# Kernel optimization log

Hardware: AMD Instinct MI355X
Metric: run time of the kernel (lower is better)

## Reference

```python
import jax, jax.numpy as jnp
import numpy as np


def setup_inputs() -> dict:
    key = jax.random.key(0)
    ks = jax.random.split(key, 5)
    B, S, H, F, E = 2, 2048, 768, 1536, 8
    scale_h = 1.0 / np.sqrt(H)
    scale_f = 1.0 / np.sqrt(F)
    return {
        "hidden_states": jax.random.normal(ks[0], (B, S, H), dtype=jnp.float32),
        "gate_w": jax.random.normal(ks[1], (E, H), dtype=jnp.float32) * scale_h,
        "w1": jax.random.normal(ks[2], (E, F, H), dtype=jnp.float32) * scale_h,
        "w3": jax.random.normal(ks[3], (E, F, H), dtype=jnp.float32) * scale_h,
        "w2": jax.random.normal(ks[4], (E, H, F), dtype=jnp.float32) * scale_f,
        "k": 2,
    }


def reference(hidden_states, gate_w, w1, w3, w2, k):
    B, S, H = hidden_states.shape
    E = gate_w.shape[0]
    x = hidden_states.reshape(-1, H)                     # [T, H]
    T = x.shape[0]

    # Router: softmax in fp32, top-k, renormalize among selected experts.
    router_logits = x @ gate_w.T                         # [T, E]
    probs = jax.nn.softmax(router_logits.astype(jnp.float32), axis=-1)
    top_w, top_i = jax.lax.top_k(probs, k)               # [T, k]
    top_w = top_w / jnp.sum(top_w, axis=-1, keepdims=True)
    top_w = top_w.astype(x.dtype)

    # Scatter top-k weights into dense [T, E] combine weights (0 for unselected).
    combine = jnp.zeros((T, E), dtype=x.dtype)
    combine = combine.at[jnp.arange(T)[:, None], top_i].set(top_w)

    # SwiGLU experts (zero-weight experts contribute exactly 0 to the sum).
    g = jnp.einsum("th,efh->tef", x, w1)                 # [T, E, F]
    u = jnp.einsum("th,efh->tef", x, w3)                 # [T, E, F]
    act = jax.nn.silu(g) * u                             # [T, E, F]
    expert_out = jnp.einsum("tef,ehf->teh", act, w2)     # [T, E, H]
    y = jnp.einsum("te,teh->th", combine, expert_out)    # [T, H]

    return y.reshape(B, S, H), router_logits
```

## Files before the change

### kernel.cpp

```cpp
#include <hip/hip_runtime.h>
#include <hip/hip_bf16.h>

#define T_TOK 4096
#define H_DIM 768
#define E_NUM 8
#define F_DIM 1536
#define WELEM (E_NUM * F_DIM * H_DIM)

typedef __bf16 bf16x8 __attribute__((ext_vector_type(8)));
typedef float f32x4 __attribute__((ext_vector_type(4)));
typedef unsigned int u32;

#define VMCNT(n) asm volatile("s_waitcnt vmcnt(" #n ")" ::: "memory")
#define CFENCE() asm volatile("" ::: "memory")

__device__ __forceinline__ unsigned short f2bf(float f) {
    unsigned int u = __float_as_uint(f);
    u += 0x7FFF + ((u >> 16) & 1);
    return (unsigned short)(u >> 16);
}

__device__ __forceinline__ void gload16(const unsigned short* g, unsigned short* l) {
    __builtin_amdgcn_global_load_lds(
        (const __attribute__((address_space(1))) u32*)(g),
        (__attribute__((address_space(3))) u32*)(l),
        16, 0, 0);
}

__global__ void convert3_kernel(const float* __restrict__ s0,
                                const float* __restrict__ s1,
                                const float* __restrict__ s2,
                                unsigned short* __restrict__ d0,
                                unsigned short* __restrict__ d1,
                                unsigned short* __restrict__ d2) {
    int i = (blockIdx.x * blockDim.x + threadIdx.x) * 4;
    int stride = gridDim.x * blockDim.x * 4;
    for (; i < 3 * WELEM; i += stride) {
        int r = i / WELEM;
        int j = i - r * WELEM;
        const float* s = (r == 0) ? s0 : (r == 1) ? s1 : s2;
        unsigned short* d = (r == 0) ? d0 : (r == 1) ? d1 : d2;
        float4 v = *reinterpret_cast<const float4*>(s + j);
        ushort4 o;
        o.x = f2bf(v.x); o.y = f2bf(v.y); o.z = f2bf(v.z); o.w = f2bf(v.w);
        *reinterpret_cast<ushort4*>(d + j) = o;
    }
}

__global__ __launch_bounds__(256) void router_kernel(
    const float* __restrict__ x,
    const float* __restrict__ gw,
    float* __restrict__ logits_out,
    float* __restrict__ weight,
    int* __restrict__ eidx,
    unsigned short* __restrict__ xb) {
    int t = blockIdx.x * 4 + (threadIdx.x >> 6);
    int lane = threadIdx.x & 63;

    const float4* xr = reinterpret_cast<const float4*>(x + (size_t)t * H_DIM);
    float4 xv[3];
#pragma unroll
    for (int i = 0; i < 3; ++i) xv[i] = xr[i * 64 + lane];

    unsigned short* xbr = xb + (size_t)t * H_DIM;
#pragma unroll
    for (int i = 0; i < 3; ++i) {
        ushort4 o;
        o.x = f2bf(xv[i].x); o.y = f2bf(xv[i].y);
        o.z = f2bf(xv[i].z); o.w = f2bf(xv[i].w);
        *reinterpret_cast<ushort4*>(xbr + (i * 64 + lane) * 4) = o;
    }

    float v[E_NUM];
#pragma unroll
    for (int e = 0; e < E_NUM; ++e) {
        const float4* g = reinterpret_cast<const float4*>(gw + e * H_DIM);
        float p = 0.f;
#pragma unroll
        for (int i = 0; i < 3; ++i) {
            float4 gv = g[i * 64 + lane];
            p += xv[i].x * gv.x + xv[i].y * gv.y + xv[i].z * gv.z + xv[i].w * gv.w;
        }
        v[e] = p;
    }
#pragma unroll
    for (int d = 1; d < 8; d <<= 1)
#pragma unroll
        for (int e = 0; e < E_NUM; ++e) v[e] += __shfl_xor(v[e], d);
    int me = lane & 7;
    float le = v[0];
#pragma unroll
    for (int e = 1; e < E_NUM; ++e) le = (me == e) ? v[e] : le;
#pragma unroll
    for (int d = 8; d < 64; d <<= 1) le += __shfl_xor(le, d);

    if (lane < 8) logits_out[t * E_NUM + lane] = le;

    float m0 = le;
#pragma unroll
    for (int d = 1; d < 8; d <<= 1) m0 = fmaxf(m0, __shfl_xor(m0, d));
    unsigned long long b0 = __ballot(le == m0);
    int e0 = (__ffsll((long long)b0) - 1) & 7;
    float le1 = (me == e0) ? -3.4e38f : le;
    float m1 = le1;
#pragma unroll
    for (int d = 1; d < 8; d <<= 1) m1 = fmaxf(m1, __shfl_xor(m1, d));
    unsigned long long b1 = __ballot(le1 == m1);
    int e1 = (__ffsll((long long)b1) - 1) & 7;

    if (lane == 0) {
        float w0 = 1.f / (1.f + __expf(m1 - m0));
        weight[t * 2 + 0] = w0;
        weight[t * 2 + 1] = 1.f - w0;
        eidx[t] = e0 | (e1 << 8);
    }
}

__global__ __launch_bounds__(256) void build_lists_kernel(
    const int* __restrict__ eidx,
    int* __restrict__ list,
    int* __restrict__ counts) {
    int e = blockIdx.x;
    int tid = threadIdx.x;
    int lane = tid & 63;
    int wv = tid >> 6;
    __shared__ int wsum[4];
    __shared__ int wbase[4];
    __shared__ int sbase;
    if (tid == 0) sbase = 0;
    __syncthreads();
    for (int c = 0; c < T_TOK; c += 256) {
        int tok = c + tid;
        int pk = eidx[tok];
        int slot = -1;
        if ((pk & 255) == e) slot = tok * 2;
        else if ((pk >> 8) == e) slot = tok * 2 + 1;
        unsigned long long m = __ballot(slot >= 0);
        int prefix = __popcll(m & ((1ull << lane) - 1ull));
        if (lane == 0) wsum[wv] = __popcll(m);
        __syncthreads();
        if (tid == 0) {
            int s = sbase;
#pragma unroll
            for (int i = 0; i < 4; ++i) { wbase[i] = s; s += wsum[i]; }
            sbase = s;
        }
        __syncthreads();
        if (slot >= 0) list[e * T_TOK + wbase[wv] + prefix] = slot;
        __syncthreads();
    }
    if (tid == 0) counts[e] = sbase;
}

__global__ __launch_bounds__(256, 3) void gemm13_kernel(
    const unsigned short* __restrict__ xb,
    const unsigned short* __restrict__ w1b,
    const unsigned short* __restrict__ w3b,
    const int* __restrict__ list,
    const int* __restrict__ counts,
    unsigned short* __restrict__ act) {
    int orig = blockIdx.x;
    int wg = (orig & 7) * 768 + (orig >> 3);
    int tm = wg & 31;
    int tn = (wg >> 5) % 24;
    int e = wg / (32 * 24);

    int cnt = counts[e];
    if (tm * 128 >= cnt) return;
    const int* lst = list + e * T_TOK + tm * 128;
    int mrem = cnt - tm * 128;

    __shared__ unsigned short sA[3][128 * 32];
    __shared__ unsigned short sB1[3][64 * 32];
    __shared__ unsigned short sB3[3][64 * 32];

    int tid = threadIdx.x;
    int lane = tid & 63;
    int wid = tid >> 6;

    int r0 = tid >> 2;
    int r1 = r0 + 64;
    int c8 = ((tid & 3) ^ ((r0 >> 1) & 3)) * 8;
    int tok0 = lst[(r0 < mrem) ? r0 : 0] >> 1;
    int tok1 = lst[(r1 < mrem) ? r1 : 0] >> 1;
    const unsigned short* gA0 = xb + (size_t)tok0 * H_DIM + c8;
    const unsigned short* gA1 = xb + (size_t)tok1 * H_DIM + c8;
    const unsigned short* gB1 = w1b + ((size_t)e * F_DIM + tn * 64 + r0) * H_DIM + c8;
    const unsigned short* gB3 = w3b + ((size_t)e * F_DIM + tn * 64 + r0) * H_DIM + c8;

    auto stage = [&](int b, int kt) {
        gload16(gA0 + kt, &sA[b][wid * 512]);
        gload16(gA1 + kt, &sA[b][2048 + wid * 512]);
        gload16(gB1 + kt, &sB1[b][wid * 512]);
        gload16(gB3 + kt, &sB3[b][wid * 512]);
    };

    int wr = (wid >> 1) * 64;
    int wc = (wid & 1) * 32;
    int fr = lane & 15;
    int kb = ((lane >> 4) ^ ((lane >> 1) & 3)) * 8;

    f32x4 accG[4][2] = {};
    f32x4 accU[4][2] = {};

    const int NT = H_DIM / 32;
    stage(0, 0);
    stage(1, 32);
    VMCNT(4);
    __builtin_amdgcn_s_barrier();
    CFENCE();
    int cur = 0;
    for (int t = 0; t < NT; ++t) {
        if (t + 2 < NT) {
            int nb = cur + 2; if (nb >= 3) nb -= 3;
            stage(nb, (t + 2) * 32);
        }
        CFENCE();

        bf16x8 a[4], b1[2], b3[2];
#pragma unroll
        for (int mi = 0; mi < 4; ++mi)
            a[mi] = *reinterpret_cast<const bf16x8*>(&sA[cur][(wr + mi * 16 + fr) * 32 + kb]);
#pragma unroll
        for (int ni = 0; ni < 2; ++ni) {
            b1[ni] = *reinterpret_cast<const bf16x8*>(&sB1[cur][(wc + ni * 16 + fr) * 32 + kb]);
            b3[ni] = *reinterpret_cast<const bf16x8*>(&sB3[cur][(wc + ni * 16 + fr) * 32 + kb]);
        }
#pragma unroll
        for (int mi = 0; mi < 4; ++mi)
#pragma unroll
            for (int ni = 0; ni < 2; ++ni) {
                accG[mi][ni] = __builtin_amdgcn_mfma_f32_16x16x32_bf16(a[mi], b1[ni], accG[mi][ni], 0, 0, 0);
                accU[mi][ni] = __builtin_amdgcn_mfma_f32_16x16x32_bf16(a[mi], b3[ni], accU[mi][ni], 0, 0, 0);
            }
        CFENCE();
        if (t + 2 < NT) { VMCNT(4); } else { VMCNT(0); }
        __builtin_amdgcn_s_barrier();
        CFENCE();
        cur = (cur + 1 < 3) ? cur + 1 : 0;
    }

    int rg = (lane >> 4) * 4;
    int ci = lane & 15;
#pragma unroll
    for (int mi = 0; mi < 4; ++mi) {
#pragma unroll
        for (int r = 0; r < 4; ++r) {
            int m = wr + mi * 16 + rg + r;
            if (m >= mrem) continue;
            int entry = lst[m];
            size_t rowOff = (size_t)entry * F_DIM + tn * 64;
#pragma unroll
            for (int ni = 0; ni < 2; ++ni) {
                float g = accG[mi][ni][r];
                float u = accU[mi][ni][r];
                float s = g / (1.f + __expf(-g));
                act[rowOff + wc + ni * 16 + ci] = f2bf(s * u);
            }
        }
    }
}

__global__ __launch_bounds__(256, 3) void gemm2_kernel(
    const unsigned short* __restrict__ act,
    const unsigned short* __restrict__ w2b,
    const int* __restrict__ list,
    const int* __restrict__ counts,
    const float* __restrict__ weight,
    float* __restrict__ ybuf) {
    int orig = blockIdx.x;
    int wg = (orig & 7) * 192 + (orig >> 3);
    int tm = wg & 31;
    int tn = (wg >> 5) % 6;
    int e = wg / (32 * 6);

    int cnt = counts[e];
    if (tm * 128 >= cnt) return;
    const int* lst = list + e * T_TOK + tm * 128;
    int mrem = cnt - tm * 128;

    __shared__ unsigned short sA[3][128 * 32];
    __shared__ unsigned short sB[3][128 * 32];

    int tid = threadIdx.x;
    int lane = tid & 63;
    int wid = tid >> 6;

    int r0 = tid >> 2;
    int r1 = r0 + 64;
    int c8 = ((tid & 3) ^ ((r0 >> 1) & 3)) * 8;
    int row0 = lst[(r0 < mrem) ? r0 : 0];
    int row1 = lst[(r1 < mrem) ? r1 : 0];
    const unsigned short* gA0 = act + (size_t)row0 * F_DIM + c8;
    const unsigned short* gA1 = act + (size_t)row1 * F_DIM + c8;
    const unsigned short* gB0 = w2b + ((size_t)e * H_DIM + tn * 128 + r0) * F_DIM + c8;
    const unsigned short* gB1 = gB0 + (size_t)64 * F_DIM;

    auto stage = [&](int b, int kt) {
        gload16(gA0 + kt, &sA[b][wid * 512]);
        gload16(gA1 + kt, &sA[b][2048 + wid * 512]);
        gload16(gB0 + kt, &sB[b][wid * 512]);
        gload16(gB1 + kt, &sB[b][2048 + wid * 512]);
    };

    int wr = (wid >> 1) * 64;
    int wc = (wid & 1) * 64;
    int fr = lane & 15;
    int kb = ((lane >> 4) ^ ((lane >> 1) & 3)) * 8;

    f32x4 acc[4][4] = {};

    const int NT = F_DIM / 32;
    stage(0, 0);
    stage(1, 32);
    VMCNT(4);
    __builtin_amdgcn_s_barrier();
    CFENCE();
    int cur = 0;
    for (int t = 0; t < NT; ++t) {
        if (t + 2 < NT) {
            int nb = cur + 2; if (nb >= 3) nb -= 3;
            stage(nb, (t + 2) * 32);
        }
        CFENCE();

        bf16x8 a[4], b[4];
#pragma unroll
        for (int mi = 0; mi < 4; ++mi)
            a[mi] = *reinterpret_cast<const bf16x8*>(&sA[cur][(wr + mi * 16 + fr) * 32 + kb]);
#pragma unroll
        for (int ni = 0; ni < 4; ++ni)
            b[ni] = *reinterpret_cast<const bf16x8*>(&sB[cur][(wc + ni * 16 + fr) * 32 + kb]);
#pragma unroll
        for (int mi = 0; mi < 4; ++mi)
#pragma unroll
            for (int ni = 0; ni < 4; ++ni)
                acc[mi][ni] = __builtin_amdgcn_mfma_f32_16x16x32_bf16(a[mi], b[ni], acc[mi][ni], 0, 0, 0);
        CFENCE();
        if (t + 2 < NT) { VMCNT(4); } else { VMCNT(0); }
        __builtin_amdgcn_s_barrier();
        CFENCE();
        cur = (cur + 1 < 3) ? cur + 1 : 0;
    }

    int rg = (lane >> 4) * 4;
    int ci = lane & 15;
#pragma unroll
    for (int mi = 0; mi < 4; ++mi) {
#pragma unroll
        for (int r = 0; r < 4; ++r) {
            int m = wr + mi * 16 + rg + r;
            if (m >= mrem) continue;
            int entry = lst[m];
            float wv = weight[entry];
            size_t rowOff = (size_t)entry * H_DIM + tn * 128;
#pragma unroll
            for (int ni = 0; ni < 4; ++ni)
                ybuf[rowOff + wc + ni * 16 + ci] = acc[mi][ni][r] * wv;
        }
    }
}

__global__ void combine_kernel(const float* __restrict__ ybuf, float* __restrict__ y) {
    int v = blockIdx.x * blockDim.x + threadIdx.x;
    if (v >= T_TOK * H_DIM / 4) return;
    int t = v / (H_DIM / 4);
    int hv = v % (H_DIM / 4);
    float4 a = reinterpret_cast<const float4*>(ybuf + (size_t)(2 * t) * H_DIM)[hv];
    float4 b = reinterpret_cast<const float4*>(ybuf + (size_t)(2 * t + 1) * H_DIM)[hv];
    float4 r;
    r.x = a.x + b.x; r.y = a.y + b.y; r.z = a.z + b.z; r.w = a.w + b.w;
    reinterpret_cast<float4*>(y)[v] = r;
}

extern "C" void kernel_launch(void* const* d_in, const int* in_sizes, int n_in,
                              void* d_out, int out_size, void* d_ws, size_t ws_size,
                              hipStream_t stream) {
    const float* x  = (const float*)d_in[0];
    const float* gw = (const float*)d_in[1];
    const float* w1 = (const float*)d_in[2];
    const float* w3 = (const float*)d_in[3];
    const float* w2 = (const float*)d_in[4];

    float* y = (float*)d_out;
    float* logits_out = y + (size_t)T_TOK * H_DIM;

    char* ws = (char*)d_ws;
    size_t off = 0;
    auto alloc = [&](size_t bytes) -> char* {
        char* p = ws + off;
        off += (bytes + 255) & ~(size_t)255;
        return p;
    };
    unsigned short* xb  = (unsigned short*)alloc((size_t)T_TOK * H_DIM * 2);
    unsigned short* w1b = (unsigned short*)alloc((size_t)WELEM * 2);
    unsigned short* w3b = (unsigned short*)alloc((size_t)WELEM * 2);
    unsigned short* w2b = (unsigned short*)alloc((size_t)WELEM * 2);
    unsigned short* act = (unsigned short*)alloc((size_t)T_TOK * 2 * F_DIM * 2);
    float* ybuf   = (float*)alloc((size_t)T_TOK * 2 * H_DIM * 4);
    float* weight = (float*)alloc((size_t)T_TOK * 2 * 4);
    int* list     = (int*)alloc((size_t)E_NUM * T_TOK * 4);
    int* counts   = (int*)alloc((size_t)E_NUM * 4);
    int* eidx     = (int*)alloc((size_t)T_TOK * 4);

    convert3_kernel<<<4096, 256, 0, stream>>>(w1, w3, w2, w1b, w3b, w2b);

    router_kernel<<<T_TOK / 4, 256, 0, stream>>>(x, gw, logits_out, weight, eidx, xb);

    build_lists_kernel<<<E_NUM, 256, 0, stream>>>(eidx, list, counts);

    gemm13_kernel<<<6144, 256, 0, stream>>>(xb, w1b, w3b, list, counts, act);

    gemm2_kernel<<<1536, 256, 0, stream>>>(act, w2b, list, counts, weight, ybuf);

    combine_kernel<<<(T_TOK * H_DIM / 4 + 255) / 256, 256, 0, stream>>>(ybuf, y);
}
```

Measured before the change: 159.6 us.

## Switch GEMM pipelines to BK=64 double buffering with 8-chunk XOR swizzle

Both expert GEMM kernels move from a three-stage, K=32 LDS pipeline to a two-stage, K=64 double buffer. The LDS layout now uses a 64-wide row with an 8-way XOR swizzle, and each tile runs two MFMA sub-steps. MFMA sections are wrapped in s_setprio raises, and occupancy hints drop from 3 to 2 blocks per CU. This halves the number of barriers and loop iterations per K. In exchange, only one tile is prefetched ahead, so latency is hidden less, and occupancy is lower because more LDS is used.

```diff
diff --git a/kernel.cpp b/kernel.cpp
--- a/kernel.cpp
+++ b/kernel.cpp
@@ -152,7 +152,7 @@
     if (tid == 0) counts[e] = sbase;
 }
 
-__global__ __launch_bounds__(256, 3) void gemm13_kernel(
+__global__ __launch_bounds__(256, 2) void gemm13_kernel(
     const unsigned short* __restrict__ xb,
     const unsigned short* __restrict__ w1b,
     const unsigned short* __restrict__ w3b,
@@ -170,74 +170,90 @@
     const int* lst = list + e * T_TOK + tm * 128;
     int mrem = cnt - tm * 128;
 
-    __shared__ unsigned short sA[3][128 * 32];
-    __shared__ unsigned short sB1[3][64 * 32];
-    __shared__ unsigned short sB3[3][64 * 32];
+    __shared__ unsigned short sA[2][128 * 64];
+    __shared__ unsigned short sB1[2][64 * 64];
+    __shared__ unsigned short sB3[2][64 * 64];
 
     int tid = threadIdx.x;
     int lane = tid & 63;
     int wid = tid >> 6;
 
-    int r0 = tid >> 2;
-    int r1 = r0 + 64;
-    int c8 = ((tid & 3) ^ ((r0 >> 1) & 3)) * 8;
-    int tok0 = lst[(r0 < mrem) ? r0 : 0] >> 1;
-    int tok1 = lst[(r1 < mrem) ? r1 : 0] >> 1;
-    const unsigned short* gA0 = xb + (size_t)tok0 * H_DIM + c8;
-    const unsigned short* gA1 = xb + (size_t)tok1 * H_DIM + c8;
-    const unsigned short* gB1 = w1b + ((size_t)e * F_DIM + tn * 64 + r0) * H_DIM + c8;
-    const unsigned short* gB3 = w3b + ((size_t)e * F_DIM + tn * 64 + r0) * H_DIM + c8;
+    int rs = tid >> 3;
+    int cs = tid & 7;
+    int ra0 = rs, ra1 = rs + 32, ra2 = rs + 64, ra3 = rs + 96;
+    int tokA0 = lst[(ra0 < mrem) ? ra0 : 0] >> 1;
+    int tokA1 = lst[(ra1 < mrem) ? ra1 : 0] >> 1;
+    int tokA2 = lst[(ra2 < mrem) ? ra2 : 0] >> 1;
+    int tokA3 = lst[(ra3 < mrem) ? ra3 : 0] >> 1;
+    const unsigned short* gA0 = xb + (size_t)tokA0 * H_DIM + ((cs ^ (ra0 & 7)) << 3);
+    const unsigned short* gA1 = xb + (size_t)tokA1 * H_DIM + ((cs ^ (ra1 & 7)) << 3);
+    const unsigned short* gA2 = xb + (size_t)tokA2 * H_DIM + ((cs ^ (ra2 & 7)) << 3);
+    const unsigned short* gA3 = xb + (size_t)tokA3 * H_DIM + ((cs ^ (ra3 & 7)) << 3);
+    const unsigned short* gB1a = w1b + ((size_t)e * F_DIM + tn * 64 + ra0) * H_DIM + ((cs ^ (ra0 & 7)) << 3);
+    const unsigned short* gB1b = w1b + ((size_t)e * F_DIM + tn * 64 + ra1) * H_DIM + ((cs ^ (ra1 & 7)) << 3);
+    const unsigned short* gB3a = w3b + ((size_t)e * F_DIM + tn * 64 + ra0) * H_DIM + ((cs ^ (ra0 & 7)) << 3);
+    const unsigned short* gB3b = w3b + ((size_t)e * F_DIM + tn * 64 + ra1) * H_DIM + ((cs ^ (ra1 & 7)) << 3);
 
     auto stage = [&](int b, int kt) {
-        gload16(gA0 + kt, &sA[b][wid * 512]);
-        gload16(gA1 + kt, &sA[b][2048 + wid * 512]);
-        gload16(gB1 + kt, &sB1[b][wid * 512]);
-        gload16(gB3 + kt, &sB3[b][wid * 512]);
+        gload16(gA0 + kt, &sA[b][0 * 2048 + wid * 512]);
+        gload16(gA1 + kt, &sA[b][1 * 2048 + wid * 512]);
+        gload16(gA2 + kt, &sA[b][2 * 2048 + wid * 512]);
+        gload16(gA3 + kt, &sA[b][3 * 2048 + wid * 512]);
+        gload16(gB1a + kt, &sB1[b][0 * 2048 + wid * 512]);
+        gload16(gB1b + kt, &sB1[b][1 * 2048 + wid * 512]);
+        gload16(gB3a + kt, &sB3[b][0 * 2048 + wid * 512]);
+        gload16(gB3b + kt, &sB3[b][1 * 2048 + wid * 512]);
     };
 
     int wr = (wid >> 1) * 64;
     int wc = (wid & 1) * 32;
     int fr = lane & 15;
-    int kb = ((lane >> 4) ^ ((lane >> 1) & 3)) * 8;
+    int f7 = fr & 7;
+    int kq = lane >> 4;
 
     f32x4 accG[4][2] = {};
     f32x4 accU[4][2] = {};
 
-    const int NT = H_DIM / 32;
+    const int NT = H_DIM / 64;
     stage(0, 0);
-    stage(1, 32);
-    VMCNT(4);
+    VMCNT(0);
     __builtin_amdgcn_s_barrier();
     CFENCE();
     int cur = 0;
     for (int t = 0; t < NT; ++t) {
-        if (t + 2 < NT) {
-            int nb = cur + 2; if (nb >= 3) nb -= 3;
-            stage(nb, (t + 2) * 32);
-        }
+        if (t + 1 < NT) stage(cur ^ 1, (t + 1) * 64);
         CFENCE();
 
-        bf16x8 a[4], b1[2], b3[2];
-#pragma unroll
-        for (int mi = 0; mi < 4; ++mi)
-            a[mi] = *reinterpret_cast<const bf16x8*>(&sA[cur][(wr + mi * 16 + fr) * 32 + kb]);
-#pragma unroll
-        for (int ni = 0; ni < 2; ++ni) {
-            b1[ni] = *reinterpret_cast<const bf16x8*>(&sB1[cur][(wc + ni * 16 + fr) * 32 + kb]);
-            b3[ni] = *reinterpret_cast<const bf16x8*>(&sB3[cur][(wc + ni * 16 + fr) * 32 + kb]);
-        }
-#pragma unroll
-        for (int mi = 0; mi < 4; ++mi)
+#pragma unroll
+        for (int kh = 0; kh < 2; ++kh) {
+            int cA = kh * 4 + kq;
+            int koff = ((cA ^ f7) << 3);
+            bf16x8 a[4], b1[2], b3[2];
+#pragma unroll
+            for (int mi = 0; mi < 4; ++mi)
+                a[mi] = *reinterpret_cast<const bf16x8*>(&sA[cur][(wr + mi * 16 + fr) * 64 + koff]);
 #pragma unroll
             for (int ni = 0; ni < 2; ++ni) {
-                accG[mi][ni] = __builtin_amdgcn_mfma_f32_16x16x32_bf16(a[mi], b1[ni], accG[mi][ni], 0, 0, 0);
-                accU[mi][ni] = __builtin_amdgcn_mfma_f32_16x16x32_bf16(a[mi], b3[ni], accU[mi][ni], 0, 0, 0);
+                b1[ni] = *reinterpret_cast<const bf16x8*>(&sB1[cur][(wc + ni * 16 + fr) * 64 + koff]);
+                b3[ni] = *reinterpret_cast<const bf16x8*>(&sB3[cur][(wc + ni * 16 + fr) * 64 + koff]);
             }
+            __builtin_amdgcn_s_setprio(1);
+#pragma unroll
+            for (int mi = 0; mi < 4; ++mi)
+#pragma unroll
+                for (int ni = 0; ni < 2; ++ni) {
+                    accG[mi][ni] = __builtin_amdgcn_mfma_f32_16x16x32_bf16(a[mi], b1[ni], accG[mi][ni], 0, 0, 0);
+                    accU[mi][ni] = __builtin_amdgcn_mfma_f32_16x16x32_bf16(a[mi], b3[ni], accU[mi][ni], 0, 0, 0);
+                }
+            __builtin_amdgcn_s_setprio(0);
+        }
         CFENCE();
-        if (t + 2 < NT) { VMCNT(4); } else { VMCNT(0); }
-        __builtin_amdgcn_s_barrier();
-        CFENCE();
-        cur = (cur + 1 < 3) ? cur + 1 : 0;
+        if (t + 1 < NT) {
+            VMCNT(0);
+            __builtin_amdgcn_s_barrier();
+            CFENCE();
+        }
+        cur ^= 1;
     }
 
     int rg = (lane >> 4) * 4;
@@ -261,7 +277,7 @@
     }
 }
 
-__global__ __launch_bounds__(256, 3) void gemm2_kernel(
+__global__ __launch_bounds__(256, 2) void gemm2_kernel(
     const unsigned short* __restrict__ act,
     const unsigned short* __restrict__ w2b,
     const int* __restrict__ list,
@@ -279,68 +295,84 @@
     const int* lst = list + e * T_TOK + tm * 128;
     int mrem = cnt - tm * 128;
 
-    __shared__ unsigned short sA[3][128 * 32];
-    __shared__ unsigned short sB[3][128 * 32];
+    __shared__ unsigned short sA[2][128 * 64];
+    __shared__ unsigned short sB[2][128 * 64];
 
     int tid = threadIdx.x;
     int lane = tid & 63;
     int wid = tid >> 6;
 
-    int r0 = tid >> 2;
-    int r1 = r0 + 64;
-    int c8 = ((tid & 3) ^ ((r0 >> 1) & 3)) * 8;
-    int row0 = lst[(r0 < mrem) ? r0 : 0];
-    int row1 = lst[(r1 < mrem) ? r1 : 0];
-    const unsigned short* gA0 = act + (size_t)row0 * F_DIM + c8;
-    const unsigned short* gA1 = act + (size_t)row1 * F_DIM + c8;
-    const unsigned short* gB0 = w2b + ((size_t)e * H_DIM + tn * 128 + r0) * F_DIM + c8;
-    const unsigned short* gB1 = gB0 + (size_t)64 * F_DIM;
+    int rs = tid >> 3;
+    int cs = tid & 7;
+    int ra0 = rs, ra1 = rs + 32, ra2 = rs + 64, ra3 = rs + 96;
+    int rowA0 = lst[(ra0 < mrem) ? ra0 : 0];
+    int rowA1 = lst[(ra1 < mrem) ? ra1 : 0];
+    int rowA2 = lst[(ra2 < mrem) ? ra2 : 0];
+    int rowA3 = lst[(ra3 < mrem) ? ra3 : 0];
+    const unsigned short* gA0 = act + (size_t)rowA0 * F_DIM + ((cs ^ (ra0 & 7)) << 3);
+    const unsigned short* gA1 = act + (size_t)rowA1 * F_DIM + ((cs ^ (ra1 & 7)) << 3);
+    const unsigned short* gA2 = act + (size_t)rowA2 * F_DIM + ((cs ^ (ra2 & 7)) << 3);
+    const unsigned short* gA3 = act + (size_t)rowA3 * F_DIM + ((cs ^ (ra3 & 7)) << 3);
+    const unsigned short* gB0 = w2b + ((size_t)e * H_DIM + tn * 128 + ra0) * F_DIM + ((cs ^ (ra0 & 7)) << 3);
+    const unsigned short* gB1 = w2b + ((size_t)e * H_DIM + tn * 128 + ra1) * F_DIM + ((cs ^ (ra1 & 7)) << 3);
+    const unsigned short* gB2 = w2b + ((size_t)e * H_DIM + tn * 128 + ra2) * F_DIM + ((cs ^ (ra2 & 7)) << 3);
+    const unsigned short* gB3 = w2b + ((size_t)e * H_DIM + tn * 128 + ra3) * F_DIM + ((cs ^ (ra3 & 7)) << 3);
 
     auto stage = [&](int b, int kt) {
-        gload16(gA0 + kt, &sA[b][wid * 512]);
-        gload16(gA1 + kt, &sA[b][2048 + wid * 512]);
-        gload16(gB0 + kt, &sB[b][wid * 512]);
-        gload16(gB1 + kt, &sB[b][2048 + wid * 512]);
+        gload16(gA0 + kt, &sA[b][0 * 2048 + wid * 512]);
+        gload16(gA1 + kt, &sA[b][1 * 2048 + wid * 512]);
+        gload16(gA2 + kt, &sA[b][2 * 2048 + wid * 512]);
+        gload16(gA3 + kt, &sA[b][3 * 2048 + wid * 512]);
+        gload16(gB0 + kt, &sB[b][0 * 2048 + wid * 512]);
+        gload16(gB1 + kt, &sB[b][1 * 2048 + wid * 512]);
+        gload16(gB2 + kt, &sB[b][2 * 2048 + wid * 512]);
+        gload16(gB3 + kt, &sB[b][3 * 2048 + wid * 512]);
     };
 
     int wr = (wid >> 1) * 64;
     int wc = (wid & 1) * 64;
     int fr = lane & 15;
-    int kb = ((lane >> 4) ^ ((lane >> 1) & 3)) * 8;
+    int f7 = fr & 7;
+    int kq = lane >> 4;
 
     f32x4 acc[4][4] = {};
 
-    const int NT = F_DIM / 32;
+    const int NT = F_DIM / 64;
     stage(0, 0);
-    stage(1, 32);
-    VMCNT(4);
+    VMCNT(0);
     __builtin_amdgcn_s_barrier();
     CFENCE();
     int cur = 0;
     for (int t = 0; t < NT; ++t) {
-        if (t + 2 < NT) {
-            int nb = cur + 2; if (nb >= 3) nb -= 3;
-            stage(nb, (t + 2) * 32);
-        }
+        if (t + 1 < NT) stage(cur ^ 1, (t + 1) * 64);
         CFENCE();
 
-        bf16x8 a[4], b[4];
-#pragma unroll
-        for (int mi = 0; mi < 4; ++mi)
-            a[mi] = *reinterpret_cast<const bf16x8*>(&sA[cur][(wr + mi * 16 + fr) * 32 + kb]);
-#pragma unroll
-        for (int ni = 0; ni < 4; ++ni)
-            b[ni] = *reinterpret_cast<const bf16x8*>(&sB[cur][(wc + ni * 16 + fr) * 32 + kb]);
-#pragma unroll
-        for (int mi = 0; mi < 4; ++mi)
+#pragma unroll
+        for (int kh = 0; kh < 2; ++kh) {
+            int cA = kh * 4 + kq;
+            int koff = ((cA ^ f7) << 3);
+            bf16x8 a[4], b[4];
+#pragma unroll
+            for (int mi = 0; mi < 4; ++mi)
+                a[mi] = *reinterpret_cast<const bf16x8*>(&sA[cur][(wr + mi * 16 + fr) * 64 + koff]);
 #pragma unroll
             for (int ni = 0; ni < 4; ++ni)
-                acc[mi][ni] = __builtin_amdgcn_mfma_f32_16x16x32_bf16(a[mi], b[ni], acc[mi][ni], 0, 0, 0);
+                b[ni] = *reinterpret_cast<const bf16x8*>(&sB[cur][(wc + ni * 16 + fr) * 64 + koff]);
+            __builtin_amdgcn_s_setprio(1);
+#pragma unroll
+            for (int mi = 0; mi < 4; ++mi)
+#pragma unroll
+                for (int ni = 0; ni < 4; ++ni)
+                    acc[mi][ni] = __builtin_amdgcn_mfma_f32_16x16x32_bf16(a[mi], b[ni], acc[mi][ni], 0, 0, 0);
+            __builtin_amdgcn_s_setprio(0);
+        }
         CFENCE();
-        if (t + 2 < NT) { VMCNT(4); } else { VMCNT(0); }
-        __builtin_amdgcn_s_barrier();
-        CFENCE();
-        cur = (cur + 1 < 3) ? cur + 1 : 0;
+        if (t + 1 < NT) {
+            VMCNT(0);
+            __builtin_amdgcn_s_barrier();
+            CFENCE();
+        }
+        cur ^= 1;
     }
 
     int rg = (lane >> 4) * 4;
```

After: 186.0 us. 1.17x slower.
